# Optimization experiments

Measured on AMD Instinct MI355X. Metric: run time of the kernel, lower is better.

Reference implementation:

```python
import jax, jax.numpy as jnp
import numpy as np

N_NODES = 100000
D_IN = 64
D_OUT = 64
N_EDGES = 1250000


def setup_inputs() -> dict:
    key = jax.random.key(0)
    k_x, k_e, k_wl, k_bl, k_wr = jax.random.split(key, 5)
    x = jax.random.normal(k_x, (N_NODES, D_IN), dtype=jnp.float32)
    edge_index = jax.random.randint(k_e, (2, N_EDGES), 0, N_NODES, dtype=jnp.int64)
    # SAGEConv params: lin_l (neighbor transform, with bias), lin_r (root transform, no bias)
    s_in = 1.0 / np.sqrt(D_IN)
    W_l = jax.random.uniform(k_wl, (D_IN, D_OUT), dtype=jnp.float32, minval=-s_in, maxval=s_in)
    b_l = jax.random.uniform(k_bl, (D_OUT,), dtype=jnp.float32, minval=-s_in, maxval=s_in)
    W_r = jax.random.uniform(k_wr, (D_IN, D_OUT), dtype=jnp.float32, minval=-s_in, maxval=s_in)
    return {"x": x, "edge_index": edge_index, "W_l": W_l, "b_l": b_l, "W_r": W_r}


def reference(x, edge_index, W_l, b_l, W_r):
    # PyG SAGEConv with aggr='add':
    #   out = lin_l(sum_{j in N(i)} x_j) + lin_r(x_i), then tanh
    src = edge_index[0]  # message sources (x_j)
    dst = edge_index[1]  # message targets (i)
    msg = x[src]                                             # [E, D_IN] gather
    aggr = jax.ops.segment_sum(msg, dst, num_segments=x.shape[0])  # [N, D_IN] scatter-add
    out = aggr @ W_l + b_l + x @ W_r                         # [N, D_OUT]
    return jnp.tanh(out)
```

## Files before the change

kernel.cpp:

```cpp
#include <hip/hip_runtime.h>
#include <hip/hip_bf16.h>
#include <hip/hip_fp16.h>

#define N_NODES 100000
#define D 64
#define N_EDGES 1250000

#define RB 64
#define NB 1563
#define FCAP 1536
#define SORT_CAP 1536

#define CB_SHIFT 11
#define NCB 49
#define CCAP 28672
#define FINE_PER_COARSE 32

#define CPAD 16

#define EPB 4096
#define PARTA_BLOCKS ((N_EDGES + EPB - 1) / EPB)
#define SEGS 16

#define TN 64
#define PRE_BLOCKS 1563

#define XP 72

typedef unsigned short ushort_t;
typedef _Float16 half_t;
typedef __attribute__((ext_vector_type(8))) _Float16 half8;
typedef __attribute__((ext_vector_type(4))) float floatx4;

__global__ __launch_bounds__(256) void pre_kernel(
    const float* __restrict__ x, const float* __restrict__ W_l,
    const float* __restrict__ b_l, const float* __restrict__ W_r,
    ushort_t* __restrict__ y, ushort_t* __restrict__ z, int N)
{
    __shared__ half_t sWt[128 * XP];
    __shared__ half_t sXh[TN * XP];
    int t = threadIdx.x;

    for (int i = t; i < 64 * 64; i += 256) {
        int k = i >> 6, c = i & 63;
        sWt[c * XP + k]        = (half_t)W_l[i];
        sWt[(64 + c) * XP + k] = (half_t)W_r[i];
    }

    long base = (long)blockIdx.x * TN;
    for (int i = t; i < TN * 16; i += 256) {
        int n = i >> 4, q = i & 15;
        long node = base + n;
        float4 v = make_float4(0.f, 0.f, 0.f, 0.f);
        if (node < N) v = ((const float4*)(x + node * D))[q];
        half_t* p = &sXh[n * XP + q * 4];
        p[0] = (half_t)v.x; p[1] = (half_t)v.y;
        p[2] = (half_t)v.z; p[3] = (half_t)v.w;
    }

    const int lane  = t & 63;
    const int w     = t >> 6;
    const int col16 = lane & 15;
    const int quad  = lane >> 4;

    float4 bq[4];
#pragma unroll
    for (int j = 0; j < 4; j++) bq[j] = *(const float4*)(b_l + j * 16 + quad * 4);

    __syncthreads();

    const int nrow = w * 16 + col16;
    half8 xb0 = *(half8*)&sXh[nrow * XP + quad * 8];
    half8 xb1 = *(half8*)&sXh[nrow * XP + 32 + quad * 8];

    long node = base + nrow;
    bool ok = (node < N);

#pragma unroll 2
    for (int ct = 0; ct < 8; ct++) {
        int c = ct * 16 + col16;
        half8 wa0 = *(half8*)&sWt[c * XP + quad * 8];
        half8 wa1 = *(half8*)&sWt[c * XP + 32 + quad * 8];
        floatx4 acc = {0.f, 0.f, 0.f, 0.f};
        acc = __builtin_amdgcn_mfma_f32_16x16x32_f16(wa0, xb0, acc, 0, 0, 0);
        acc = __builtin_amdgcn_mfma_f32_16x16x32_f16(wa1, xb1, acc, 0, 0, 0);

        if (ok) {
            int oc = ct * 16 + quad * 4;
            union { half_t h[4]; uint2 u; } pk;
            if (ct < 4) {
                pk.h[0] = (half_t)acc[0]; pk.h[1] = (half_t)acc[1];
                pk.h[2] = (half_t)acc[2]; pk.h[3] = (half_t)acc[3];
                *(uint2*)(y + node * D + oc) = pk.u;
            } else {
                float4 bv = bq[ct - 4];
                pk.h[0] = (half_t)(acc[0] + bv.x); pk.h[1] = (half_t)(acc[1] + bv.y);
                pk.h[2] = (half_t)(acc[2] + bv.z); pk.h[3] = (half_t)(acc[3] + bv.w);
                *(uint2*)(z + node * D + (oc - 64)) = pk.u;
            }
        }
    }
}

__global__ __launch_bounds__(256) void partA_kernel(
    const int* __restrict__ src, const int* __restrict__ dst,
    int* __restrict__ ccursor, unsigned* __restrict__ coarse, int E)
{
    __shared__ int hist[4][NCB];
    __shared__ int wbase[4][NCB];
    int t = threadIdx.x;
    const int w = t >> 6;

    if (t < 4 * NCB) ((int*)hist)[t] = 0;
    __syncthreads();

    int base = blockIdx.x * EPB;
    int lim = E - base; if (lim > EPB) lim = EPB;

    for (int i = t; i < lim; i += 256) {
        int d = dst[base + i];
        atomicAdd(&hist[w][d >> CB_SHIFT], 1);
    }
    __syncthreads();

    if (t < NCB) {
        int c0 = hist[0][t], c1 = hist[1][t];
        int c2 = hist[2][t], c3 = hist[3][t];
        int tot = c0 + c1 + c2 + c3;
        int b0 = tot ? atomicAdd(&ccursor[t * CPAD], tot) : 0;
        wbase[0][t] = b0;
        wbase[1][t] = b0 + c0;
        wbase[2][t] = b0 + c0 + c1;
        wbase[3][t] = b0 + c0 + c1 + c2;
    }
    __syncthreads();

    for (int i = t; i < lim; i += 256) {
        int d = dst[base + i];
        int s = src[base + i];
        int b = d >> CB_SHIFT;
        int pos = atomicSub(&hist[w][b], 1) - 1;
        coarse[(size_t)b * CCAP + wbase[w][b] + pos] =
            (unsigned)s | ((unsigned)(d & ((1 << CB_SHIFT) - 1)) << 17);
    }
}

__global__ __launch_bounds__(256) void partB_kernel(
    const unsigned* __restrict__ coarse, const int* __restrict__ ccursor,
    int* __restrict__ fcursor, unsigned* __restrict__ fine)
{
    __shared__ int hist[4][FINE_PER_COARSE];
    __shared__ int wbase[4][FINE_PER_COARSE];
    int cb = blockIdx.x >> 4;
    int seg = blockIdx.x & 15;
    int t = threadIdx.x;
    const int w = t >> 6;

    int cnt = ccursor[cb * CPAD];
    int segLen = (cnt + SEGS - 1) / SEGS;
    int beg = seg * segLen;
    int end = beg + segLen; if (end > cnt) end = cnt;

    if (t < 4 * FINE_PER_COARSE) ((int*)hist)[t] = 0;
    __syncthreads();

    const unsigned* __restrict__ slab = coarse + (size_t)cb * CCAP;

    for (int i = beg + t; i < end; i += 256) {
        unsigned e = slab[i];
        atomicAdd(&hist[w][(e >> 17) >> 6], 1);
    }
    __syncthreads();

    if (t < FINE_PER_COARSE) {
        int c0 = hist[0][t], c1 = hist[1][t];
        int c2 = hist[2][t], c3 = hist[3][t];
        int tot = c0 + c1 + c2 + c3;
        int fb = cb * FINE_PER_COARSE + t;
        int b0 = tot ? atomicAdd(&fcursor[fb * CPAD], tot) : 0;
        wbase[0][t] = b0;
        wbase[1][t] = b0 + c0;
        wbase[2][t] = b0 + c0 + c1;
        wbase[3][t] = b0 + c0 + c1 + c2;
    }
    __syncthreads();

    for (int i = beg + t; i < end; i += 256) {
        unsigned e = slab[i];
        unsigned cl = e >> 17;
        int fb_loc = cl >> 6;
        int pos = atomicSub(&hist[w][fb_loc], 1) - 1;
        size_t fb = (size_t)cb * FINE_PER_COARSE + fb_loc;
        fine[fb * FCAP + wbase[w][fb_loc] + pos] =
            (e & 0x1FFFFu) | ((cl & 63u) << 17);
    }
}

__global__ __launch_bounds__(512) void sortgather_kernel(
    const ushort_t* __restrict__ y, const ushort_t* __restrict__ z,
    const unsigned* __restrict__ part, const int* __restrict__ cursor,
    float* __restrict__ out, int N)
{
    __shared__ int sorted[SORT_CAP];
    __shared__ int hist[RB];
    __shared__ int cur[RB];
    __shared__ int begL[RB];

    int b = blockIdx.x;
    int t = threadIdx.x;
    int cnt = cursor[b * CPAD];
    if (cnt > SORT_CAP) cnt = SORT_CAP;
    const unsigned* __restrict__ slab = part + (size_t)b * FCAP;

    unsigned e0 = 0, e1 = 0, e2 = 0;
    int i0 = t, i1 = t + 512, i2 = t + 1024;
    if (i0 < cnt) e0 = slab[i0];
    if (i1 < cnt) e1 = slab[i1];
    if (i2 < cnt) e2 = slab[i2];

    if (t < RB) hist[t] = 0;
    __syncthreads();

    if (i0 < cnt) atomicAdd(&hist[e0 >> 17], 1);
    if (i1 < cnt) atomicAdd(&hist[e1 >> 17], 1);
    if (i2 < cnt) atomicAdd(&hist[e2 >> 17], 1);
    __syncthreads();

    if (t < RB) {
        int v = hist[t];
        int inc = v;
#pragma unroll
        for (int off = 1; off < RB; off <<= 1) {
            int n = __shfl_up(inc, off, RB);
            if (t >= off) inc += n;
        }
        int ex = inc - v;
        cur[t] = ex;
        begL[t] = ex;
    }
    __syncthreads();

    if (i0 < cnt) { int p = atomicAdd(&cur[e0 >> 17], 1); sorted[p] = (int)(e0 & 0x1FFFF); }
    if (i1 < cnt) { int p = atomicAdd(&cur[e1 >> 17], 1); sorted[p] = (int)(e1 & 0x1FFFF); }
    if (i2 < cnt) { int p = atomicAdd(&cur[e2 >> 17], 1); sorted[p] = (int)(e2 & 0x1FFFF); }
    __syncthreads();

    const int g = t >> 3;
    const int f = t & 7;
    int myBeg = begL[g];
    int myDeg = hist[g];

    float2 acc0 = make_float2(0.f, 0.f), acc1 = acc0, acc2 = acc0, acc3 = acc0;

    int i = 0;
    for (; i + 4 <= myDeg; i += 4) {
        int s0 = sorted[myBeg + i];
        int s1 = sorted[myBeg + i + 1];
        int s2 = sorted[myBeg + i + 2];
        int s3 = sorted[myBeg + i + 3];
        uint4 r0 = ((const uint4*)(y + (size_t)s0 * D))[f];
        uint4 r1 = ((const uint4*)(y + (size_t)s1 * D))[f];
        uint4 r2 = ((const uint4*)(y + (size_t)s2 * D))[f];
        uint4 r3 = ((const uint4*)(y + (size_t)s3 * D))[f];
#define ACC(r) { \
        float2 c0 = __half22float2(*(const __half2*)&(r).x); \
        float2 c1 = __half22float2(*(const __half2*)&(r).y); \
        float2 c2 = __half22float2(*(const __half2*)&(r).z); \
        float2 c3 = __half22float2(*(const __half2*)&(r).w); \
        acc0.x += c0.x; acc0.y += c0.y; acc1.x += c1.x; acc1.y += c1.y; \
        acc2.x += c2.x; acc2.y += c2.y; acc3.x += c3.x; acc3.y += c3.y; }
        ACC(r0) ACC(r1) ACC(r2) ACC(r3)
    }
    for (; i < myDeg; i++) {
        int s = sorted[myBeg + i];
        uint4 r = ((const uint4*)(y + (size_t)s * D))[f];
        ACC(r)
    }
#undef ACC

    long gn = (long)b * RB + g;
    if (gn < N) {
        uint4 zr = ((const uint4*)(z + (size_t)gn * D))[f];
        float2 z0 = __half22float2(*(const __half2*)&zr.x);
        float2 z1 = __half22float2(*(const __half2*)&zr.y);
        float2 z2 = __half22float2(*(const __half2*)&zr.z);
        float2 z3 = __half22float2(*(const __half2*)&zr.w);
        float4 o0, o1;
        o0.x = tanhf(acc0.x + z0.x); o0.y = tanhf(acc0.y + z0.y);
        o0.z = tanhf(acc1.x + z1.x); o0.w = tanhf(acc1.y + z1.y);
        o1.x = tanhf(acc2.x + z2.x); o1.y = tanhf(acc2.y + z2.y);
        o1.z = tanhf(acc3.x + z3.x); o1.w = tanhf(acc3.y + z3.y);
        float4* op = (float4*)(out + gn * D);
        op[2 * f] = o0;
        op[2 * f + 1] = o1;
    }
}

extern "C" void kernel_launch(void* const* d_in, const int* in_sizes, int n_in,
                              void* d_out, int out_size, void* d_ws, size_t ws_size,
                              hipStream_t stream) {
    const float* x   = (const float*)d_in[0];
    const int* ei    = (const int*)d_in[1];
    const float* W_l = (const float*)d_in[2];
    const float* b_l = (const float*)d_in[3];
    const float* W_r = (const float*)d_in[4];
    float* out = (float*)d_out;

    const int N = N_NODES;
    const int E = N_EDGES;
    const int* src = ei;
    const int* dst = ei + E;

    char* ws = (char*)d_ws;
    ushort_t* y      = (ushort_t*)(ws);
    ushort_t* z      = (ushort_t*)(ws + 12800000);
    unsigned* coarse = (unsigned*)(ws + 25600000);
    unsigned* fine   = (unsigned*)(ws + 31219712);
    int* ccursor     = (int*)(ws + 40822784);
    int* fcursor     = (int*)(ws + 40825920);

    hipMemsetAsync(ccursor, 0, 103168, stream);

    partA_kernel<<<PARTA_BLOCKS, 256, 0, stream>>>(src, dst, ccursor, coarse, E);
    pre_kernel<<<PRE_BLOCKS, 256, 0, stream>>>(x, W_l, b_l, W_r, y, z, N);
    partB_kernel<<<NCB * SEGS, 256, 0, stream>>>(coarse, ccursor, fcursor, fine);
    sortgather_kernel<<<NB, 512, 0, stream>>>(y, z, fine, fcursor, out, N);
}
```

Measured before the change: 166.3 us.

## Fuse partition and projection kernels; stage bucket scatters through shared memory

New measurement: 149.8 us. -9.9%, faster.

```diff
diff --git a/kernel.cpp b/kernel.cpp
--- a/kernel.cpp
+++ b/kernel.cpp
@@ -18,28 +18,104 @@
 
 #define CPAD 16
 
-#define EPB 4096
+#define EPB 8192
 #define PARTA_BLOCKS ((N_EDGES + EPB - 1) / EPB)
 #define SEGS 16
+#define SEG_CAP 1792
 
 #define TN 64
 #define PRE_BLOCKS 1563
+#define FUSED_BLOCKS (PARTA_BLOCKS + PRE_BLOCKS)
 
 #define XP 72
+
+#define SMEM_BYTES 35328
 
 typedef unsigned short ushort_t;
 typedef _Float16 half_t;
 typedef __attribute__((ext_vector_type(8))) _Float16 half8;
 typedef __attribute__((ext_vector_type(4))) float floatx4;
 
-__global__ __launch_bounds__(256) void pre_kernel(
+__global__ __launch_bounds__(256) void pre_part_kernel(
     const float* __restrict__ x, const float* __restrict__ W_l,
     const float* __restrict__ b_l, const float* __restrict__ W_r,
-    ushort_t* __restrict__ y, ushort_t* __restrict__ z, int N)
+    ushort_t* __restrict__ y, ushort_t* __restrict__ z,
+    const int* __restrict__ src, const int* __restrict__ dst,
+    int* __restrict__ ccursor, unsigned* __restrict__ coarse,
+    int N, int E)
 {
-    __shared__ half_t sWt[128 * XP];
-    __shared__ half_t sXh[TN * XP];
+    extern __shared__ char smem[];
     int t = threadIdx.x;
+
+    if (blockIdx.x < PARTA_BLOCKS) {
+        int* hist4       = (int*)smem;
+        int* lbase       = (int*)(smem + 1024);
+        int* gbase       = (int*)(smem + 1280);
+        int* lwb         = (int*)(smem + 1536);
+        unsigned* sortedL = (unsigned*)(smem + 2560);
+        const int w = t >> 6;
+
+        if (t < 4 * NCB) hist4[t] = 0;
+        __syncthreads();
+
+        int base = blockIdx.x * EPB;
+        int lim = E - base; if (lim > EPB) lim = EPB;
+
+        for (int i = t; i < lim; i += 256)
+            atomicAdd(&hist4[w * NCB + (dst[base + i] >> CB_SHIFT)], 1);
+        __syncthreads();
+
+        if (t < 64) {
+            int c0 = 0, c1 = 0, c2 = 0, c3 = 0, tot = 0;
+            if (t < NCB) {
+                c0 = hist4[t]; c1 = hist4[NCB + t];
+                c2 = hist4[2 * NCB + t]; c3 = hist4[3 * NCB + t];
+                tot = c0 + c1 + c2 + c3;
+            }
+            int inc = tot;
+#pragma unroll
+            for (int off = 1; off < 64; off <<= 1) {
+                int n = __shfl_up(inc, off, 64);
+                if (t >= off) inc += n;
+            }
+            int ex = inc - tot;
+            if (t < NCB) {
+                lbase[t] = ex;
+                gbase[t] = tot ? atomicAdd(&ccursor[t * CPAD], tot) : 0;
+                lwb[t]           = ex;
+                lwb[NCB + t]     = ex + c0;
+                lwb[2 * NCB + t] = ex + c0 + c1;
+                lwb[3 * NCB + t] = ex + c0 + c1 + c2;
+            } else {
+                lbase[t] = lim;
+            }
+        }
+        __syncthreads();
+
+        for (int i = t; i < lim; i += 256) {
+            int d = dst[base + i];
+            int s = src[base + i];
+            int b = d >> CB_SHIFT;
+            int pos = atomicSub(&hist4[w * NCB + b], 1) - 1;
+            sortedL[lwb[w * NCB + b] + pos] =
+                (unsigned)s | ((unsigned)(d & ((1 << CB_SHIFT) - 1)) << 17);
+        }
+        __syncthreads();
+
+        for (int i = t; i < lim; i += 256) {
+            int lo = 0;
+#pragma unroll
+            for (int s2 = 32; s2; s2 >>= 1) {
+                int c = lo + s2;
+                if (c < 64 && lbase[c] <= i) lo = c;
+            }
+            coarse[(size_t)lo * CCAP + gbase[lo] + (i - lbase[lo])] = sortedL[i];
+        }
+        return;
+    }
+
+    half_t* sWt = (half_t*)smem;
+    half_t* sXh = (half_t*)(smem + 18432);
 
     for (int i = t; i < 64 * 64; i += 256) {
         int k = i >> 6, c = i & 63;
@@ -47,7 +123,7 @@
         sWt[(64 + c) * XP + k] = (half_t)W_r[i];
     }
 
-    long base = (long)blockIdx.x * TN;
+    long base = (long)(blockIdx.x - PARTA_BLOCKS) * TN;
     for (int i = t; i < TN * 16; i += 256) {
         int n = i >> 4, q = i & 15;
         long node = base + n;
@@ -57,91 +133,63 @@
         p[0] = (half_t)v.x; p[1] = (half_t)v.y;
         p[2] = (half_t)v.z; p[3] = (half_t)v.w;
     }
+    __syncthreads();
 
     const int lane  = t & 63;
     const int w     = t >> 6;
     const int col16 = lane & 15;
     const int quad  = lane >> 4;
 
-    float4 bq[4];
-#pragma unroll
-    for (int j = 0; j < 4; j++) bq[j] = *(const float4*)(b_l + j * 16 + quad * 4);
-
-    __syncthreads();
-
     const int nrow = w * 16 + col16;
     half8 xb0 = *(half8*)&sXh[nrow * XP + quad * 8];
     half8 xb1 = *(half8*)&sXh[nrow * XP + 32 + quad * 8];
 
-    long node = base + nrow;
-    bool ok = (node < N);
-
-#pragma unroll 2
-    for (int ct = 0; ct < 8; ct++) {
+    float4 bq[4];
+#pragma unroll
+    for (int j = 0; j < 4; j++) bq[j] = *(const float4*)(b_l + j * 16 + quad * 4);
+
+#pragma unroll
+    for (int ct = 0; ct < 4; ct++) {
         int c = ct * 16 + col16;
         half8 wa0 = *(half8*)&sWt[c * XP + quad * 8];
         half8 wa1 = *(half8*)&sWt[c * XP + 32 + quad * 8];
         floatx4 acc = {0.f, 0.f, 0.f, 0.f};
         acc = __builtin_amdgcn_mfma_f32_16x16x32_f16(wa0, xb0, acc, 0, 0, 0);
         acc = __builtin_amdgcn_mfma_f32_16x16x32_f16(wa1, xb1, acc, 0, 0, 0);
-
-        if (ok) {
-            int oc = ct * 16 + quad * 4;
-            union { half_t h[4]; uint2 u; } pk;
-            if (ct < 4) {
-                pk.h[0] = (half_t)acc[0]; pk.h[1] = (half_t)acc[1];
-                pk.h[2] = (half_t)acc[2]; pk.h[3] = (half_t)acc[3];
-                *(uint2*)(y + node * D + oc) = pk.u;
-            } else {
-                float4 bv = bq[ct - 4];
-                pk.h[0] = (half_t)(acc[0] + bv.x); pk.h[1] = (half_t)(acc[1] + bv.y);
-                pk.h[2] = (half_t)(acc[2] + bv.z); pk.h[3] = (half_t)(acc[3] + bv.w);
-                *(uint2*)(z + node * D + (oc - 64)) = pk.u;
-            }
-        }
-    }
-}
-
-__global__ __launch_bounds__(256) void partA_kernel(
-    const int* __restrict__ src, const int* __restrict__ dst,
-    int* __restrict__ ccursor, unsigned* __restrict__ coarse, int E)
-{
-    __shared__ int hist[4][NCB];
-    __shared__ int wbase[4][NCB];
-    int t = threadIdx.x;
-    const int w = t >> 6;
-
-    if (t < 4 * NCB) ((int*)hist)[t] = 0;
-    __syncthreads();
-
-    int base = blockIdx.x * EPB;
-    int lim = E - base; if (lim > EPB) lim = EPB;
-
-    for (int i = t; i < lim; i += 256) {
-        int d = dst[base + i];
-        atomicAdd(&hist[w][d >> CB_SHIFT], 1);
-    }
-    __syncthreads();
-
-    if (t < NCB) {
-        int c0 = hist[0][t], c1 = hist[1][t];
-        int c2 = hist[2][t], c3 = hist[3][t];
-        int tot = c0 + c1 + c2 + c3;
-        int b0 = tot ? atomicAdd(&ccursor[t * CPAD], tot) : 0;
-        wbase[0][t] = b0;
-        wbase[1][t] = b0 + c0;
-        wbase[2][t] = b0 + c0 + c1;
-        wbase[3][t] = b0 + c0 + c1 + c2;
-    }
-    __syncthreads();
-
-    for (int i = t; i < lim; i += 256) {
-        int d = dst[base + i];
-        int s = src[base + i];
-        int b = d >> CB_SHIFT;
-        int pos = atomicSub(&hist[w][b], 1) - 1;
-        coarse[(size_t)b * CCAP + wbase[w][b] + pos] =
-            (unsigned)s | ((unsigned)(d & ((1 << CB_SHIFT) - 1)) << 17);
+        union { half_t h[4]; uint2 u; } pk;
+        pk.h[0] = (half_t)acc[0]; pk.h[1] = (half_t)acc[1];
+        pk.h[2] = (half_t)acc[2]; pk.h[3] = (half_t)acc[3];
+        *(uint2*)&sXh[(w * 16 + col16) * XP + ct * 16 + quad * 4] = pk.u;
+    }
+    __syncthreads();
+
+    for (int c2 = t; c2 < TN * 8; c2 += 256) {
+        int row = c2 >> 3, f = c2 & 7;
+        if (base + row < N)
+            *(uint4*)(y + (base + row) * D + f * 8) = *(uint4*)&sXh[row * XP + f * 8];
+    }
+    __syncthreads();
+
+#pragma unroll
+    for (int ct = 4; ct < 8; ct++) {
+        int c = ct * 16 + col16;
+        half8 wa0 = *(half8*)&sWt[c * XP + quad * 8];
+        half8 wa1 = *(half8*)&sWt[c * XP + 32 + quad * 8];
+        floatx4 acc = {0.f, 0.f, 0.f, 0.f};
+        acc = __builtin_amdgcn_mfma_f32_16x16x32_f16(wa0, xb0, acc, 0, 0, 0);
+        acc = __builtin_amdgcn_mfma_f32_16x16x32_f16(wa1, xb1, acc, 0, 0, 0);
+        float4 bv = bq[ct - 4];
+        union { half_t h[4]; uint2 u; } pk;
+        pk.h[0] = (half_t)(acc[0] + bv.x); pk.h[1] = (half_t)(acc[1] + bv.y);
+        pk.h[2] = (half_t)(acc[2] + bv.z); pk.h[3] = (half_t)(acc[3] + bv.w);
+        *(uint2*)&sXh[(w * 16 + col16) * XP + (ct - 4) * 16 + quad * 4] = pk.u;
+    }
+    __syncthreads();
+
+    for (int c2 = t; c2 < TN * 8; c2 += 256) {
+        int row = c2 >> 3, f = c2 & 7;
+        if (base + row < N)
+            *(uint4*)(z + (base + row) * D + f * 8) = *(uint4*)&sXh[row * XP + f * 8];
     }
 }
 
@@ -149,8 +197,12 @@
     const unsigned* __restrict__ coarse, const int* __restrict__ ccursor,
     int* __restrict__ fcursor, unsigned* __restrict__ fine)
 {
-    __shared__ int hist[4][FINE_PER_COARSE];
-    __shared__ int wbase[4][FINE_PER_COARSE];
+    __shared__ int hist4[4 * FINE_PER_COARSE];
+    __shared__ int lbase2[FINE_PER_COARSE];
+    __shared__ int gbase2[FINE_PER_COARSE];
+    __shared__ int lwb2[4 * FINE_PER_COARSE];
+    __shared__ unsigned sortedL[SEG_CAP];
+
     int cb = blockIdx.x >> 4;
     int seg = blockIdx.x & 15;
     int t = threadIdx.x;
@@ -160,39 +212,62 @@
     int segLen = (cnt + SEGS - 1) / SEGS;
     int beg = seg * segLen;
     int end = beg + segLen; if (end > cnt) end = cnt;
-
-    if (t < 4 * FINE_PER_COARSE) ((int*)hist)[t] = 0;
-    __syncthreads();
-
-    const unsigned* __restrict__ slab = coarse + (size_t)cb * CCAP;
-
-    for (int i = beg + t; i < end; i += 256) {
-        unsigned e = slab[i];
-        atomicAdd(&hist[w][(e >> 17) >> 6], 1);
-    }
-    __syncthreads();
-
-    if (t < FINE_PER_COARSE) {
-        int c0 = hist[0][t], c1 = hist[1][t];
-        int c2 = hist[2][t], c3 = hist[3][t];
-        int tot = c0 + c1 + c2 + c3;
-        int fb = cb * FINE_PER_COARSE + t;
-        int b0 = tot ? atomicAdd(&fcursor[fb * CPAD], tot) : 0;
-        wbase[0][t] = b0;
-        wbase[1][t] = b0 + c0;
-        wbase[2][t] = b0 + c0 + c1;
-        wbase[3][t] = b0 + c0 + c1 + c2;
-    }
-    __syncthreads();
-
-    for (int i = beg + t; i < end; i += 256) {
+    int lim = end - beg; if (lim < 0) lim = 0;
+
+    if (t < 4 * FINE_PER_COARSE) hist4[t] = 0;
+    __syncthreads();
+
+    const unsigned* __restrict__ slab = coarse + (size_t)cb * CCAP + beg;
+
+    for (int i = t; i < lim; i += 256)
+        atomicAdd(&hist4[w * FINE_PER_COARSE + ((slab[i] >> 17) >> 6)], 1);
+    __syncthreads();
+
+    if (t < 64) {
+        int c0 = 0, c1 = 0, c2 = 0, c3 = 0, tot = 0;
+        if (t < FINE_PER_COARSE) {
+            c0 = hist4[t]; c1 = hist4[FINE_PER_COARSE + t];
+            c2 = hist4[2 * FINE_PER_COARSE + t]; c3 = hist4[3 * FINE_PER_COARSE + t];
+            tot = c0 + c1 + c2 + c3;
+        }
+        int inc = tot;
+#pragma unroll
+        for (int off = 1; off < 32; off <<= 1) {
+            int n = __shfl_up(inc, off, 64);
+            if (t >= off) inc += n;
+        }
+        int ex = inc - tot;
+        if (t < FINE_PER_COARSE) {
+            lbase2[t] = ex;
+            int fb = cb * FINE_PER_COARSE + t;
+            gbase2[t] = tot ? atomicAdd(&fcursor[fb * CPAD], tot) : 0;
+            lwb2[t]                       = ex;
+            lwb2[FINE_PER_COARSE + t]     = ex + c0;
+            lwb2[2 * FINE_PER_COARSE + t] = ex + c0 + c1;
+            lwb2[3 * FINE_PER_COARSE + t] = ex + c0 + c1 + c2;
+        }
+    }
+    __syncthreads();
+
+    for (int i = t; i < lim; i += 256) {
         unsigned e = slab[i];
         unsigned cl = e >> 17;
-        int fb_loc = cl >> 6;
-        int pos = atomicSub(&hist[w][fb_loc], 1) - 1;
-        size_t fb = (size_t)cb * FINE_PER_COARSE + fb_loc;
-        fine[fb * FCAP + wbase[w][fb_loc] + pos] =
+        int loc = cl >> 6;
+        int pos = atomicSub(&hist4[w * FINE_PER_COARSE + loc], 1) - 1;
+        sortedL[lwb2[w * FINE_PER_COARSE + loc] + pos] =
             (e & 0x1FFFFu) | ((cl & 63u) << 17);
+    }
+    __syncthreads();
+
+    for (int i = t; i < lim; i += 256) {
+        int lo = 0;
+#pragma unroll
+        for (int s2 = 16; s2; s2 >>= 1) {
+            int c = lo + s2;
+            if (c < FINE_PER_COARSE && lbase2[c] <= i) lo = c;
+        }
+        fine[((size_t)cb * FINE_PER_COARSE + lo) * FCAP + gbase2[lo] + (i - lbase2[lo])]
+            = sortedL[i];
     }
 }
 
@@ -321,8 +396,8 @@
 
     hipMemsetAsync(ccursor, 0, 103168, stream);
 
-    partA_kernel<<<PARTA_BLOCKS, 256, 0, stream>>>(src, dst, ccursor, coarse, E);
-    pre_kernel<<<PRE_BLOCKS, 256, 0, stream>>>(x, W_l, b_l, W_r, y, z, N);
+    pre_part_kernel<<<FUSED_BLOCKS, 256, SMEM_BYTES, stream>>>(
+        x, W_l, b_l, W_r, y, z, src, dst, ccursor, coarse, N, E);
     partB_kernel<<<NCB * SEGS, 256, 0, stream>>>(coarse, ccursor, fcursor, fine);
     sortgather_kernel<<<NB, 512, 0, stream>>>(y, z, fine, fcursor, out, N);
 }
```

## Fuse single-pass edge partition with node transform into one kernel

Applied to the files above, without the earlier changes.

Measured after the change: 146.1 us. 12.1% less time.

```diff
diff --git a/kernel.cpp b/kernel.cpp
--- a/kernel.cpp
+++ b/kernel.cpp
@@ -11,35 +11,68 @@
 #define FCAP 1536
 #define SORT_CAP 1536
 
-#define CB_SHIFT 11
-#define NCB 49
-#define CCAP 28672
-#define FINE_PER_COARSE 32
-
 #define CPAD 16
 
-#define EPB 4096
-#define PARTA_BLOCKS ((N_EDGES + EPB - 1) / EPB)
-#define SEGS 16
+#define EPB 8192
+#define PART_BLOCKS ((N_EDGES + EPB - 1) / EPB)
 
 #define TN 64
 #define PRE_BLOCKS 1563
+#define FUSED_BLOCKS (PART_BLOCKS + PRE_BLOCKS)
 
 #define XP 72
+
+#define SMEM_BYTES 27648
 
 typedef unsigned short ushort_t;
 typedef _Float16 half_t;
 typedef __attribute__((ext_vector_type(8))) _Float16 half8;
 typedef __attribute__((ext_vector_type(4))) float floatx4;
 
-__global__ __launch_bounds__(256) void pre_kernel(
+__global__ __launch_bounds__(256) void pre_part_kernel(
     const float* __restrict__ x, const float* __restrict__ W_l,
     const float* __restrict__ b_l, const float* __restrict__ W_r,
-    ushort_t* __restrict__ y, ushort_t* __restrict__ z, int N)
+    ushort_t* __restrict__ y, ushort_t* __restrict__ z,
+    const int* __restrict__ src, const int* __restrict__ dst,
+    int* __restrict__ fcursor, unsigned* __restrict__ fine,
+    int N, int E)
 {
-    __shared__ half_t sWt[128 * XP];
-    __shared__ half_t sXh[TN * XP];
+    extern __shared__ char smem[];
     int t = threadIdx.x;
+
+    if (blockIdx.x < PART_BLOCKS) {
+        int* hist  = (int*)smem;
+        int* gbase = (int*)(smem + 6400);
+
+        for (int i = t; i < NB; i += 256) hist[i] = 0;
+        __syncthreads();
+
+        int base = blockIdx.x * EPB;
+        int lim = E - base; if (lim > EPB) lim = EPB;
+
+        for (int i = t; i < lim; i += 256)
+            atomicAdd(&hist[dst[base + i] >> 6], 1);
+        __syncthreads();
+
+        for (int b = t; b < NB; b += 256) {
+            int c = hist[b];
+            gbase[b] = c ? atomicAdd(&fcursor[b * CPAD], c) : 0;
+        }
+        __syncthreads();
+
+        for (int i = t; i < lim; i += 256) {
+            int d = dst[base + i];
+            int s = src[base + i];
+            int bin = d >> 6;
+            int pos = atomicSub(&hist[bin], 1) - 1;
+            fine[(size_t)bin * FCAP + gbase[bin] + pos] =
+                (unsigned)s | ((unsigned)(d & 63) << 17);
+        }
+        return;
+    }
+
+    half_t* sWt = (half_t*)smem;
+    half_t* sXh = (half_t*)(smem + 18432);
 
     for (int i = t; i < 64 * 64; i += 256) {
         int k = i >> 6, c = i & 63;
@@ -47,7 +80,7 @@
         sWt[(64 + c) * XP + k] = (half_t)W_r[i];
     }
 
-    long base = (long)blockIdx.x * TN;
+    long base = (long)(blockIdx.x - PART_BLOCKS) * TN;
     for (int i = t; i < TN * 16; i += 256) {
         int n = i >> 4, q = i & 15;
         long node = base + n;
@@ -57,142 +90,63 @@
         p[0] = (half_t)v.x; p[1] = (half_t)v.y;
         p[2] = (half_t)v.z; p[3] = (half_t)v.w;
     }
+    __syncthreads();
 
     const int lane  = t & 63;
     const int w     = t >> 6;
     const int col16 = lane & 15;
     const int quad  = lane >> 4;
 
-    float4 bq[4];
-#pragma unroll
-    for (int j = 0; j < 4; j++) bq[j] = *(const float4*)(b_l + j * 16 + quad * 4);
-
-    __syncthreads();
-
     const int nrow = w * 16 + col16;
     half8 xb0 = *(half8*)&sXh[nrow * XP + quad * 8];
     half8 xb1 = *(half8*)&sXh[nrow * XP + 32 + quad * 8];
 
-    long node = base + nrow;
-    bool ok = (node < N);
-
-#pragma unroll 2
-    for (int ct = 0; ct < 8; ct++) {
+    float4 bq[4];
+#pragma unroll
+    for (int j = 0; j < 4; j++) bq[j] = *(const float4*)(b_l + j * 16 + quad * 4);
+
+#pragma unroll
+    for (int ct = 0; ct < 4; ct++) {
         int c = ct * 16 + col16;
         half8 wa0 = *(half8*)&sWt[c * XP + quad * 8];
         half8 wa1 = *(half8*)&sWt[c * XP + 32 + quad * 8];
         floatx4 acc = {0.f, 0.f, 0.f, 0.f};
         acc = __builtin_amdgcn_mfma_f32_16x16x32_f16(wa0, xb0, acc, 0, 0, 0);
         acc = __builtin_amdgcn_mfma_f32_16x16x32_f16(wa1, xb1, acc, 0, 0, 0);
-
-        if (ok) {
-            int oc = ct * 16 + quad * 4;
-            union { half_t h[4]; uint2 u; } pk;
-            if (ct < 4) {
-                pk.h[0] = (half_t)acc[0]; pk.h[1] = (half_t)acc[1];
-                pk.h[2] = (half_t)acc[2]; pk.h[3] = (half_t)acc[3];
-                *(uint2*)(y + node * D + oc) = pk.u;
-            } else {
-                float4 bv = bq[ct - 4];
-                pk.h[0] = (half_t)(acc[0] + bv.x); pk.h[1] = (half_t)(acc[1] + bv.y);
-                pk.h[2] = (half_t)(acc[2] + bv.z); pk.h[3] = (half_t)(acc[3] + bv.w);
-                *(uint2*)(z + node * D + (oc - 64)) = pk.u;
-            }
-        }
-    }
-}
-
-__global__ __launch_bounds__(256) void partA_kernel(
-    const int* __restrict__ src, const int* __restrict__ dst,
-    int* __restrict__ ccursor, unsigned* __restrict__ coarse, int E)
-{
-    __shared__ int hist[4][NCB];
-    __shared__ int wbase[4][NCB];
-    int t = threadIdx.x;
-    const int w = t >> 6;
-
-    if (t < 4 * NCB) ((int*)hist)[t] = 0;
-    __syncthreads();
-
-    int base = blockIdx.x * EPB;
-    int lim = E - base; if (lim > EPB) lim = EPB;
-
-    for (int i = t; i < lim; i += 256) {
-        int d = dst[base + i];
-        atomicAdd(&hist[w][d >> CB_SHIFT], 1);
-    }
-    __syncthreads();
-
-    if (t < NCB) {
-        int c0 = hist[0][t], c1 = hist[1][t];
-        int c2 = hist[2][t], c3 = hist[3][t];
-        int tot = c0 + c1 + c2 + c3;
-        int b0 = tot ? atomicAdd(&ccursor[t * CPAD], tot) : 0;
-        wbase[0][t] = b0;
-        wbase[1][t] = b0 + c0;
-        wbase[2][t] = b0 + c0 + c1;
-        wbase[3][t] = b0 + c0 + c1 + c2;
-    }
-    __syncthreads();
-
-    for (int i = t; i < lim; i += 256) {
-        int d = dst[base + i];
-        int s = src[base + i];
-        int b = d >> CB_SHIFT;
-        int pos = atomicSub(&hist[w][b], 1) - 1;
-        coarse[(size_t)b * CCAP + wbase[w][b] + pos] =
-            (unsigned)s | ((unsigned)(d & ((1 << CB_SHIFT) - 1)) << 17);
-    }
-}
-
-__global__ __launch_bounds__(256) void partB_kernel(
-    const unsigned* __restrict__ coarse, const int* __restrict__ ccursor,
-    int* __restrict__ fcursor, unsigned* __restrict__ fine)
-{
-    __shared__ int hist[4][FINE_PER_COARSE];
-    __shared__ int wbase[4][FINE_PER_COARSE];
-    int cb = blockIdx.x >> 4;
-    int seg = blockIdx.x & 15;
-    int t = threadIdx.x;
-    const int w = t >> 6;
-
-    int cnt = ccursor[cb * CPAD];
-    int segLen = (cnt + SEGS - 1) / SEGS;
-    int beg = seg * segLen;
-    int end = beg + segLen; if (end > cnt) end = cnt;
-
-    if (t < 4 * FINE_PER_COARSE) ((int*)hist)[t] = 0;
-    __syncthreads();
-
-    const unsigned* __restrict__ slab = coarse + (size_t)cb * CCAP;
-
-    for (int i = beg + t; i < end; i += 256) {
-        unsigned e = slab[i];
-        atomicAdd(&hist[w][(e >> 17) >> 6], 1);
-    }
-    __syncthreads();
-
-    if (t < FINE_PER_COARSE) {
-        int c0 = hist[0][t], c1 = hist[1][t];
-        int c2 = hist[2][t], c3 = hist[3][t];
-        int tot = c0 + c1 + c2 + c3;
-        int fb = cb * FINE_PER_COARSE + t;
-        int b0 = tot ? atomicAdd(&fcursor[fb * CPAD], tot) : 0;
-        wbase[0][t] = b0;
-        wbase[1][t] = b0 + c0;
-        wbase[2][t] = b0 + c0 + c1;
-        wbase[3][t] = b0 + c0 + c1 + c2;
-    }
-    __syncthreads();
-
-    for (int i = beg + t; i < end; i += 256) {
-        unsigned e = slab[i];
-        unsigned cl = e >> 17;
-        int fb_loc = cl >> 6;
-        int pos = atomicSub(&hist[w][fb_loc], 1) - 1;
-        size_t fb = (size_t)cb * FINE_PER_COARSE + fb_loc;
-        fine[fb * FCAP + wbase[w][fb_loc] + pos] =
-            (e & 0x1FFFFu) | ((cl & 63u) << 17);
+        union { half_t h[4]; uint2 u; } pk;
+        pk.h[0] = (half_t)acc[0]; pk.h[1] = (half_t)acc[1];
+        pk.h[2] = (half_t)acc[2]; pk.h[3] = (half_t)acc[3];
+        *(uint2*)&sXh[(w * 16 + col16) * XP + ct * 16 + quad * 4] = pk.u;
+    }
+    __syncthreads();
+
+    for (int c2 = t; c2 < TN * 8; c2 += 256) {
+        int row = c2 >> 3, f = c2 & 7;
+        if (base + row < N)
+            *(uint4*)(y + (base + row) * D + f * 8) = *(uint4*)&sXh[row * XP + f * 8];
+    }
+    __syncthreads();
+
+#pragma unroll
+    for (int ct = 4; ct < 8; ct++) {
+        int c = ct * 16 + col16;
+        half8 wa0 = *(half8*)&sWt[c * XP + quad * 8];
+        half8 wa1 = *(half8*)&sWt[c * XP + 32 + quad * 8];
+        floatx4 acc = {0.f, 0.f, 0.f, 0.f};
+        acc = __builtin_amdgcn_mfma_f32_16x16x32_f16(wa0, xb0, acc, 0, 0, 0);
+        acc = __builtin_amdgcn_mfma_f32_16x16x32_f16(wa1, xb1, acc, 0, 0, 0);
+        float4 bv = bq[ct - 4];
+        union { half_t h[4]; uint2 u; } pk;
+        pk.h[0] = (half_t)(acc[0] + bv.x); pk.h[1] = (half_t)(acc[1] + bv.y);
+        pk.h[2] = (half_t)(acc[2] + bv.z); pk.h[3] = (half_t)(acc[3] + bv.w);
+        *(uint2*)&sXh[(w * 16 + col16) * XP + (ct - 4) * 16 + quad * 4] = pk.u;
+    }
+    __syncthreads();
+
+    for (int c2 = t; c2 < TN * 8; c2 += 256) {
+        int row = c2 >> 3, f = c2 & 7;
+        if (base + row < N)
+            *(uint4*)(z + (base + row) * D + f * 8) = *(uint4*)&sXh[row * XP + f * 8];
     }
 }
 
@@ -312,17 +266,14 @@
     const int* dst = ei + E;
 
     char* ws = (char*)d_ws;
-    ushort_t* y      = (ushort_t*)(ws);
-    ushort_t* z      = (ushort_t*)(ws + 12800000);
-    unsigned* coarse = (unsigned*)(ws + 25600000);
-    unsigned* fine   = (unsigned*)(ws + 31219712);
-    int* ccursor     = (int*)(ws + 40822784);
-    int* fcursor     = (int*)(ws + 40825920);
-
-    hipMemsetAsync(ccursor, 0, 103168, stream);
-
-    partA_kernel<<<PARTA_BLOCKS, 256, 0, stream>>>(src, dst, ccursor, coarse, E);
-    pre_kernel<<<PRE_BLOCKS, 256, 0, stream>>>(x, W_l, b_l, W_r, y, z, N);
-    partB_kernel<<<NCB * SEGS, 256, 0, stream>>>(coarse, ccursor, fcursor, fine);
+    ushort_t* y    = (ushort_t*)(ws);
+    ushort_t* z    = (ushort_t*)(ws + 12800000);
+    unsigned* fine = (unsigned*)(ws + 25600000);
+    int* fcursor   = (int*)(ws + 35203072);
+
+    hipMemsetAsync(fcursor, 0, 100032, stream);
+
+    pre_part_kernel<<<FUSED_BLOCKS, 256, SMEM_BYTES, stream>>>(
+        x, W_l, b_l, W_r, y, z, src, dst, fcursor, fine, N, E);
     sortgather_kernel<<<NB, 512, 0, stream>>>(y, z, fine, fcursor, out, N);
 }
```
